# Performance work log

Measured on AMD Instinct MI355X. Metric: run time of the kernel, lower is better.

## Reference

```python
import math
import jax, jax.numpy as jnp
import numpy as np

B, T, C, H = 4, 2048, 1024, 16
HS = C // H


def setup_inputs() -> dict:
    key = jax.random.key(0)
    ks = jax.random.split(key, 5)
    s_in = 1.0 / math.sqrt(C)
    return {
        "x": jax.random.normal(ks[0], (B, T, C), dtype=jnp.float32),
        "w_attn": jax.random.normal(ks[1], (C, 3 * C), dtype=jnp.float32) * s_in,
        "b_attn": jax.random.normal(ks[2], (3 * C,), dtype=jnp.float32) * 0.02,
        "w_proj": jax.random.normal(ks[3], (C, C), dtype=jnp.float32) * s_in,
        "b_proj": jax.random.normal(ks[4], (C,), dtype=jnp.float32) * 0.02,
    }


def reference(x, w_attn, b_attn, w_proj, b_proj):
    Bx, Tx, Cx = x.shape
    hs = Cx // H
    qkv = x @ w_attn + b_attn  # [B, T, 3C]
    q, k, v = jnp.split(qkv, 3, axis=-1)
    # [B, H, T, hs]
    q = q.reshape(Bx, Tx, H, hs).transpose(0, 2, 1, 3)
    k = k.reshape(Bx, Tx, H, hs).transpose(0, 2, 1, 3)
    v = v.reshape(Bx, Tx, H, hs).transpose(0, 2, 1, 3)
    scale = 1.0 / math.sqrt(hs)
    att = jnp.einsum("bhqd,bhkd->bhqk", q, k) * scale  # [B, H, T, T]
    causal = jnp.tril(jnp.ones((Tx, Tx), dtype=bool))
    att = jnp.where(causal, att, -jnp.inf)
    att = jax.nn.softmax(att, axis=-1)
    y = jnp.einsum("bhqk,bhkd->bhqd", att, v)  # [B, H, T, hs]
    y = y.transpose(0, 2, 1, 3).reshape(Bx, Tx, Cx)
    return y @ w_proj + b_proj
```

## Files before the change

kernel.cpp:

```cpp
#include <hip/hip_runtime.h>
#include <stdint.h>

#define Bn 4
#define Tn 2048
#define Cn 1024
#define Hn 16
#define HSn 64
#define Mn (Bn*Tn)
#define N1n (3*Cn)

typedef unsigned short u16;
typedef unsigned int u32;
typedef __attribute__((ext_vector_type(8))) short short8;
typedef __attribute__((ext_vector_type(4))) float f32x4;
typedef __attribute__((ext_vector_type(16))) float f32x16;

__device__ __forceinline__ u16 f2bf(float f){
  u32 u = __float_as_uint(f);
  u += 0x7fffu + ((u >> 16) & 1u);
  return (u16)(u >> 16);
}

__device__ __forceinline__ u32 pkbf(float lo, float hi_){
  u32 r; asm("v_cvt_pk_bf16_f32 %0, %1, %2" : "=v"(r) : "v"(lo), "v"(hi_)); return r;
}

__device__ __forceinline__ float fexp2(float x){
  float r; asm("v_exp_f32 %0, %1" : "=v"(r) : "v"(x)); return r;
}

__device__ __forceinline__ void plswap(u32 &a, u32 &b){
  auto r = __builtin_amdgcn_permlane32_swap(a, b, false, false);
  a = r[0]; b = r[1];
}

__device__ __forceinline__ void gload_lds16(const void* g, void* l){
  __builtin_amdgcn_global_load_lds(
      (const __attribute__((address_space(1))) u32*)g,
      (__attribute__((address_space(3))) u32*)l, 16, 0, 0);
}

#define BARRIER() __builtin_amdgcn_s_barrier()
#define CFENCE() asm volatile("" ::: "memory")

__global__ void k_cvt(const float* __restrict__ in, u16* __restrict__ out, int n8){
  int i = blockIdx.x*256 + threadIdx.x;
  if (i >= n8) return;
  const float4* p = (const float4*)(in) + (size_t)i*2;
  float4 a = p[0], b = p[1];
  uint4 r;
  r.x = (u32)f2bf(a.x) | ((u32)f2bf(a.y) << 16);
  r.y = (u32)f2bf(a.z) | ((u32)f2bf(a.w) << 16);
  r.z = (u32)f2bf(b.x) | ((u32)f2bf(b.y) << 16);
  r.w = (u32)f2bf(b.z) | ((u32)f2bf(b.w) << 16);
  *((uint4*)(out) + i) = r;
}

__global__ void k_tcvt(const float* __restrict__ in, u16* __restrict__ out, int R, int Cc){
  __shared__ float sh[64][68];
  int tid = threadIdx.x;
  int c0 = blockIdx.x*64, r0 = blockIdx.y*64;
  int rr = tid >> 4, c4 = (tid & 15) * 4;
  #pragma unroll
  for (int p=0;p<4;p++){
    int r = rr + 16*p;
    *(float4*)&sh[r][c4] = *(const float4*)&in[(size_t)(r0+r)*Cc + c0 + c4];
  }
  __syncthreads();
  #pragma unroll
  for (int p=0;p<4;p++){
    int oc = rr + 16*p;
    u32 w0 = (u32)f2bf(sh[c4+0][oc]) | ((u32)f2bf(sh[c4+1][oc]) << 16);
    u32 w1 = (u32)f2bf(sh[c4+2][oc]) | ((u32)f2bf(sh[c4+3][oc]) << 16);
    uint2 pk; pk.x = w0; pk.y = w1;
    *(uint2*)&out[(size_t)(c0+oc)*R + r0 + c4] = pk;
  }
}

template <int MODE>
__global__ __launch_bounds__(512, 1)
void k_gemm1p(const u16* __restrict__ A, const u16* __restrict__ Bt,
              const float* __restrict__ bias, void* __restrict__ Cout,
              u16* __restrict__ vt, int Nn_)
{
  extern __shared__ char smem[];
  const int nkt = 16;
  int tid = threadIdx.x;
  int wave = tid >> 6, lane = tid & 63, g = lane >> 4, cl = lane & 15;
  int wm = wave >> 1, wn = wave & 1;

  int blk = blockIdx.x;
  int by = ((blk & 7) << 2) + ((blk >> 3) & 3);
  int bx = ((blk >> 5) & 7) + ((blk >> 8) << 3);
  int m0 = by * 256, n0 = bx * 128;

  int srow = tid >> 3;
  int scolb = (tid & 7) << 4;
  int ssw = scolb ^ ((srow & 7) << 4);
  const char* Agp = (const char*)A  + (size_t)(m0 + srow) * 2048 + ssw;
  const char* Bgp = (const char*)Bt + (size_t)(n0 + srow) * 2048 + ssw;

  #define STAGE6(t_) { int bb_ = (t_)%3; \
    char* ab_ = smem + bb_*32768 + (wave<<10); \
    const char* ag_ = Agp + (size_t)(t_)*128; \
    gload_lds16(ag_,          ab_); \
    gload_lds16(ag_+131072,   ab_+8192); \
    gload_lds16(ag_+262144,   ab_+16384); \
    gload_lds16(ag_+393216,   ab_+24576); \
    char* bbp_ = smem + 98304 + bb_*16384 + (wave<<10); \
    const char* bg_ = Bgp + (size_t)(t_)*128; \
    gload_lds16(bg_,          bbp_); \
    gload_lds16(bg_+131072,   bbp_+8192); }

  f32x4 acc[4][4];
  #pragma unroll
  for (int i=0;i<4;i++)
    #pragma unroll
    for (int j=0;j<4;j++) acc[i][j] = (f32x4){0.f,0.f,0.f,0.f};

  STAGE6(0);
  STAGE6(1);
  asm volatile("s_waitcnt vmcnt(6)" ::: "memory");
  BARRIER(); CFENCE();

  for (int t=0; t<nkt; ++t){
    if (t+2 < nkt){
      STAGE6(t+2);
      asm volatile("s_waitcnt vmcnt(6)" ::: "memory");
    } else {
      asm volatile("s_waitcnt vmcnt(0)" ::: "memory");
    }
    const char* Asb = smem + (t%3)*32768;
    const char* Bsb = smem + 98304 + (t%3)*16384;
    short8 a[4][2], bq[4][2];
    #pragma unroll
    for (int i=0;i<4;i++){
      int row = wm*64 + i*16 + cl;
      #pragma unroll
      for (int ks=0;ks<2;ks++)
        a[i][ks] = *(const short8*)(Asb + row*128 + ((ks*64 + g*16) ^ ((row&7)<<4)));
    }
    #pragma unroll
    for (int j=0;j<4;j++){
      int row = wn*64 + j*16 + cl;
      #pragma unroll
      for (int ks=0;ks<2;ks++)
        bq[j][ks] = *(const short8*)(Bsb + row*128 + ((ks*64 + g*16) ^ ((row&7)<<4)));
    }
    __builtin_amdgcn_s_setprio(1);
    #pragma unroll
    for (int ks=0;ks<2;ks++)
      #pragma unroll
      for (int i=0;i<4;i++)
        #pragma unroll
        for (int j=0;j<4;j++)
          acc[i][j] = __builtin_amdgcn_mfma_f32_16x16x32_bf16(a[i][ks], bq[j][ks], acc[i][j], 0, 0, 0);
    __builtin_amdgcn_s_setprio(0);
    CFENCE(); BARRIER(); CFENCE();
  }
  #undef STAGE6

  #pragma unroll
  for (int jj=0;jj<4;jj++){
    int col = n0 + wn*64 + jj*16 + cl;
    float bj = bias[col];
    if (MODE == 0){
      #pragma unroll
      for (int i=0;i<4;i++){
        int rowb = m0 + wm*64 + i*16 + g*4;
        #pragma unroll
        for (int r=0;r<4;r++)
          ((float*)Cout)[(size_t)(rowb+r)*Nn_ + col] = acc[i][jj][r] + bj;
      }
    } else if (col < 2*Cn){
      #pragma unroll
      for (int i=0;i<4;i++){
        int rowb = m0 + wm*64 + i*16 + g*4;
        #pragma unroll
        for (int r=0;r<4;r++)
          ((u16*)Cout)[(size_t)(rowb+r)*Nn_ + col] = f2bf(acc[i][jj][r] + bj);
      }
    } else {
      int hd = col - 2*Cn;
      #pragma unroll
      for (int i=0;i<4;i++){
        int rowb = m0 + wm*64 + i*16 + g*4;
        int bb = rowb >> 11, tt = rowb & 2047;
        u16* dst = vt + (((size_t)(bb*16 + (hd>>6)))*64 + (hd&63))*2048 + tt;
        uint2 pk;
        pk.x = (u32)f2bf(acc[i][jj][0]+bj) | ((u32)f2bf(acc[i][jj][1]+bj) << 16);
        pk.y = (u32)f2bf(acc[i][jj][2]+bj) | ((u32)f2bf(acc[i][jj][3]+bj) << 16);
        *(uint2*)dst = pk;
      }
    }
  }
}

__global__ __launch_bounds__(256, 4)
void k_attn(const u16* __restrict__ qkv, const u16* __restrict__ vt, u16* __restrict__ yb){
  __shared__ __align__(16) u16 Ks[2][64*64];
  __shared__ __align__(16) u16 Vs[2][64*64];
  int tid = threadIdx.x, wave = tid >> 6, lane = tid & 63;
  int ql = lane & 31, hi = lane >> 5;
  int blk = blockIdx.x;
  int xcd = blk & 7, rest = blk >> 3;
  int bh  = xcd + 8*(rest & 7);
  int qt  = 15 - (rest >> 3);
  int b = bh >> 4, h = bh & 15;

  const u16* Kbase = qkv + (size_t)b*Tn*N1n + Cn + h*HSn;
  const u16* Vbase = vt  + (size_t)bh*HSn*Tn;

  auto STAGE = [&](int bufi, int kt){
    int kb_ = kt*64;
    #pragma unroll
    for (int it=0; it<2; ++it){
      int off = it*4096 + tid*16;
      int row = off >> 7;
      int cb  = off & 127;
      int gc  = (cb ^ ((row & 7) << 4)) >> 1;
      gload_lds16(Kbase + (size_t)(kb_ + row)*N1n + gc,
                  (char*)&Ks[bufi][0] + it*4096 + (wave << 10));
      gload_lds16(Vbase + (size_t)row*Tn + kb_ + gc,
                  (char*)&Vs[bufi][0] + it*4096 + (wave << 10));
    }
  };

  const float QSC = 0.125f * 1.44269504f;

  int q0 = qt * 128;
  int qw0 = q0 + wave*32;
  int qg  = qw0 + ql;
  int ntiles = 2*qt + 2;

  const u16* Qp = qkv + (size_t)(b*Tn + qg)*N1n + h*HSn;
  short8 qf[4];
  #pragma unroll
  for (int dc=0; dc<4; ++dc){
    union { short8 v; u32 w[4]; } qa;
    qa.v = *(const short8*)&Qp[dc*16 + hi*8];
    #pragma unroll
    for (int t=0; t<4; ++t){
      u32 w = qa.w[t];
      float lo = __uint_as_float(w << 16);
      float hf = __uint_as_float(w & 0xffff0000u);
      qa.w[t] = pkbf(lo*QSC, hf*QSC);
    }
    qf[dc] = qa.v;
  }

  f32x16 accO[2];
  #pragma unroll
  for (int f=0; f<2; ++f)
    #pragma unroll
    for (int r=0; r<16; ++r) accO[f][r] = 0.f;
  float m_ = -1e30f, l_ = 0.f;

  STAGE(0, 0);
  asm volatile("s_waitcnt vmcnt(0)" ::: "memory");
  __syncthreads();
  int buf = 0;

  for (int kt=0; kt<ntiles; ++kt){
    if (kt+1 < ntiles) STAGE(buf^1, kt+1);
    const char* Ksb = (const char*)&Ks[buf][0];
    const char* Vsb = (const char*)&Vs[buf][0];
    #pragma unroll
    for (int ksub=0; ksub<2; ++ksub){
      int kbase = kt*64 + ksub*32;
      if (kbase <= qw0 + 31){
        f32x16 s;
        #pragma unroll
        for (int r=0; r<16; ++r) s[r] = 0.f;
        __builtin_amdgcn_s_setprio(1);
        #pragma unroll
        for (int dc=0; dc<4; ++dc){
          short8 kf = *(const short8*)(Ksb + ((ksub*32 + ql) << 7)
                          + ((dc*32 + hi*16) ^ ((ql & 7) << 4)));
          s = __builtin_amdgcn_mfma_f32_32x32x16_bf16(kf, qf[dc], s, 0, 0, 0);
        }
        __builtin_amdgcn_s_setprio(0);
        float p[16];
        if (kbase + 31 > qw0){
          #pragma unroll
          for (int r=0; r<16; ++r){
            int krow = kbase + (r&3) + 8*(r>>2) + 4*hi;
            p[r] = (krow > qg) ? -1e30f : s[r];
          }
        } else {
          #pragma unroll
          for (int r=0; r<16; ++r) p[r] = s[r];
        }
        float t0 = fmaxf(fmaxf(fmaxf(p[0],p[1]),fmaxf(p[2],p[3])),
                         fmaxf(fmaxf(p[4],p[5]),fmaxf(p[6],p[7])));
        float t1 = fmaxf(fmaxf(fmaxf(p[8],p[9]),fmaxf(p[10],p[11])),
                         fmaxf(fmaxf(p[12],p[13]),fmaxf(p[14],p[15])));
        float tm = fmaxf(t0, t1);
        { u32 ua = __float_as_uint(tm), ub = ua; plswap(ua, ub);
          tm = fmaxf(__uint_as_float(ua), __uint_as_float(ub)); }
        if (!__all(tm - m_ <= 8.0f)){
          float mn = fmaxf(m_, tm);
          float al = fexp2(m_ - mn);
          m_ = mn; l_ *= al;
          #pragma unroll
          for (int f=0; f<2; ++f)
            #pragma unroll
            for (int r=0; r<16; ++r) accO[f][r] *= al;
        }
        float ls = 0.f;
        #pragma unroll
        for (int r=0; r<16; ++r){ float e = fexp2(p[r] - m_); p[r] = e; ls += e; }
        { u32 ua = __float_as_uint(ls), ub = ua; plswap(ua, ub);
          l_ += __uint_as_float(ua) + __uint_as_float(ub); }
        #pragma unroll
        for (int ks=0; ks<2; ++ks){
          int pb = ks*8;
          u32 w0 = pkbf(p[pb+0], p[pb+1]);
          u32 w1 = pkbf(p[pb+2], p[pb+3]);
          u32 w2 = pkbf(p[pb+4], p[pb+5]);
          u32 w3 = pkbf(p[pb+6], p[pb+7]);
          plswap(w0, w2);
          plswap(w1, w3);
          union { u32 w[4]; short8 v; } pu;
          pu.w[0] = w0; pu.w[1] = w1; pu.w[2] = w2; pu.w[3] = w3;
          __builtin_amdgcn_s_setprio(1);
          #pragma unroll
          for (int f=0; f<2; ++f){
            short8 vf = *(const short8*)(Vsb + ((f*32 + ql) << 7)
                            + ((ksub*64 + ks*32 + hi*16) ^ ((ql & 7) << 4)));
            accO[f] = __builtin_amdgcn_mfma_f32_32x32x16_bf16(vf, pu.v, accO[f], 0, 0, 0);
          }
          __builtin_amdgcn_s_setprio(0);
        }
      }
    }
    asm volatile("s_waitcnt vmcnt(0)" ::: "memory");
    __syncthreads();
    buf ^= 1;
  }

  float rl = 1.0f / l_;
  u16* yp = yb + (size_t)(b*Tn + qg)*Cn + h*HSn;
  #pragma unroll
  for (int f=0; f<2; ++f)
    #pragma unroll
    for (int rq=0; rq<4; ++rq){
      int d0 = f*32 + rq*8 + hi*4;
      float v0 = accO[f][rq*4+0]*rl, v1 = accO[f][rq*4+1]*rl;
      float v2 = accO[f][rq*4+2]*rl, v3 = accO[f][rq*4+3]*rl;
      uint2 pk2;
      pk2.x = (u32)f2bf(v0) | ((u32)f2bf(v1) << 16);
      pk2.y = (u32)f2bf(v2) | ((u32)f2bf(v3) << 16);
      *(uint2*)&yp[d0] = pk2;
    }
}

extern "C" void kernel_launch(void* const* d_in, const int* in_sizes, int n_in,
                              void* d_out, int out_size, void* d_ws, size_t ws_size,
                              hipStream_t stream)
{
  const float* x      = (const float*)d_in[0];
  const float* w_attn = (const float*)d_in[1];
  const float* b_attn = (const float*)d_in[2];
  const float* w_proj = (const float*)d_in[3];
  const float* b_proj = (const float*)d_in[4];
  float* out = (float*)d_out;
  char* ws = (char*)d_ws;

  size_t off = 0;
  u16* xb  = (u16*)(ws + off); off += (size_t)Mn*Cn*2;
  u16* waT = (u16*)(ws + off); off += (size_t)N1n*Cn*2;
  u16* wpT = (u16*)(ws + off); off += (size_t)Cn*Cn*2;
  u16* qkv = (u16*)(ws + off); off += (size_t)Mn*N1n*2;
  u16* vt  = (u16*)(ws + off); off += (size_t)Bn*Hn*HSn*Tn*2;
  u16* yb  = (u16*)(ws + off); off += (size_t)Mn*Cn*2;

  (void)hipFuncSetAttribute((const void*)k_gemm1p<1>,
        hipFuncAttributeMaxDynamicSharedMemorySize, 147456);
  (void)hipFuncSetAttribute((const void*)k_gemm1p<0>,
        hipFuncAttributeMaxDynamicSharedMemorySize, 147456);

  k_cvt<<<dim3(Mn*Cn/8/256), 256, 0, stream>>>(x, xb, Mn*Cn/8);
  k_tcvt<<<dim3(N1n/64, Cn/64), 256, 0, stream>>>(w_attn, waT, Cn, N1n);
  k_tcvt<<<dim3(Cn/64, Cn/64), 256, 0, stream>>>(w_proj, wpT, Cn, Cn);
  k_gemm1p<1><<<dim3((Mn/256)*(N1n/128)), 512, 147456, stream>>>(xb, waT, b_attn, qkv, vt, N1n);
  k_attn<<<dim3(1024), 256, 0, stream>>>(qkv, vt, yb);
  k_gemm1p<0><<<dim3((Mn/256)*(Cn/128)), 512, 147456, stream>>>(yb, wpT, b_proj, out, nullptr, Cn);
}
```

Measured before the change: 156.7 us.

## Switch GEMMs to 128x128 tiles, 256 threads, double buffering, XCD-aware block mapping

Both GEMMs move from 256x128 tiles on 512-thread blocks with a triple-buffered 144KB LDS pipeline to 128x128 tiles on 256-thread blocks. These use a double-buffered 64KB LDS layout with two blocks per CU. Block indices are remapped so that each XCD owns a contiguous range of M-tiles, which aims for L2 locality, and the grid becomes twice as large. The goal is better occupancy and tail balance, at the cost of a shallower prefetch pipeline, an extra barrier per k-step, and lower per-block data reuse.

```diff
diff --git a/kernel.cpp b/kernel.cpp
--- a/kernel.cpp
+++ b/kernel.cpp
@@ -78,10 +78,10 @@
 }
 
 template <int MODE>
-__global__ __launch_bounds__(512, 1)
-void k_gemm1p(const u16* __restrict__ A, const u16* __restrict__ Bt,
-              const float* __restrict__ bias, void* __restrict__ Cout,
-              u16* __restrict__ vt, int Nn_)
+__global__ __launch_bounds__(256, 2)
+void k_gemm2(const u16* __restrict__ A, const u16* __restrict__ Bt,
+             const float* __restrict__ bias, void* __restrict__ Cout,
+             u16* __restrict__ vt, int Nn_, int byPerXcd)
 {
   extern __shared__ char smem[];
   const int nkt = 16;
@@ -89,10 +89,10 @@
   int wave = tid >> 6, lane = tid & 63, g = lane >> 4, cl = lane & 15;
   int wm = wave >> 1, wn = wave & 1;
 
-  int blk = blockIdx.x;
-  int by = ((blk & 7) << 2) + ((blk >> 3) & 3);
-  int bx = ((blk >> 5) & 7) + ((blk >> 8) << 3);
-  int m0 = by * 256, n0 = bx * 128;
+  int xcd = blockIdx.x & 7, idx = blockIdx.x >> 3;
+  int by = xcd * byPerXcd + (idx % byPerXcd);
+  int bx = idx / byPerXcd;
+  int m0 = by * 128, n0 = bx * 128;
 
   int srow = tid >> 3;
   int scolb = (tid & 7) << 4;
@@ -100,17 +100,19 @@
   const char* Agp = (const char*)A  + (size_t)(m0 + srow) * 2048 + ssw;
   const char* Bgp = (const char*)Bt + (size_t)(n0 + srow) * 2048 + ssw;
 
-  #define STAGE6(t_) { int bb_ = (t_)%3; \
-    char* ab_ = smem + bb_*32768 + (wave<<10); \
-    const char* ag_ = Agp + (size_t)(t_)*128; \
-    gload_lds16(ag_,          ab_); \
-    gload_lds16(ag_+131072,   ab_+8192); \
-    gload_lds16(ag_+262144,   ab_+16384); \
-    gload_lds16(ag_+393216,   ab_+24576); \
-    char* bbp_ = smem + 98304 + bb_*16384 + (wave<<10); \
-    const char* bg_ = Bgp + (size_t)(t_)*128; \
-    gload_lds16(bg_,          bbp_); \
-    gload_lds16(bg_+131072,   bbp_+8192); }
+  #define STG(t_, b_) { \
+    const char* ag = Agp + (size_t)(t_)*128; \
+    const char* bg = Bgp + (size_t)(t_)*128; \
+    char* ab = smem + (b_)*32768 + (wave<<10); \
+    char* bb = ab + 16384; \
+    gload_lds16(ag,          ab); \
+    gload_lds16(ag+ 65536,   ab+4096); \
+    gload_lds16(ag+131072,   ab+8192); \
+    gload_lds16(ag+196608,   ab+12288); \
+    gload_lds16(bg,          bb); \
+    gload_lds16(bg+ 65536,   bb+4096); \
+    gload_lds16(bg+131072,   bb+8192); \
+    gload_lds16(bg+196608,   bb+12288); }
 
   f32x4 acc[4][4];
   #pragma unroll
@@ -118,20 +120,19 @@
     #pragma unroll
     for (int j=0;j<4;j++) acc[i][j] = (f32x4){0.f,0.f,0.f,0.f};
 
-  STAGE6(0);
-  STAGE6(1);
-  asm volatile("s_waitcnt vmcnt(6)" ::: "memory");
-  BARRIER(); CFENCE();
+  STG(0, 0);
 
   for (int t=0; t<nkt; ++t){
-    if (t+2 < nkt){
-      STAGE6(t+2);
-      asm volatile("s_waitcnt vmcnt(6)" ::: "memory");
+    int b = t & 1;
+    if (t+1 < nkt){
+      STG(t+1, b^1);
+      asm volatile("s_waitcnt vmcnt(8)" ::: "memory");
     } else {
       asm volatile("s_waitcnt vmcnt(0)" ::: "memory");
     }
-    const char* Asb = smem + (t%3)*32768;
-    const char* Bsb = smem + 98304 + (t%3)*16384;
+    BARRIER(); CFENCE();
+    const char* Asb = smem + b*32768;
+    const char* Bsb = Asb + 16384;
     short8 a[4][2], bq[4][2];
     #pragma unroll
     for (int i=0;i<4;i++){
@@ -147,6 +148,7 @@
       for (int ks=0;ks<2;ks++)
         bq[j][ks] = *(const short8*)(Bsb + row*128 + ((ks*64 + g*16) ^ ((row&7)<<4)));
     }
+    asm volatile("s_waitcnt lgkmcnt(0)" ::: "memory");
     __builtin_amdgcn_s_setprio(1);
     #pragma unroll
     for (int ks=0;ks<2;ks++)
@@ -158,7 +160,7 @@
     __builtin_amdgcn_s_setprio(0);
     CFENCE(); BARRIER(); CFENCE();
   }
-  #undef STAGE6
+  #undef STG
 
   #pragma unroll
   for (int jj=0;jj<4;jj++){
@@ -375,15 +377,15 @@
   u16* vt  = (u16*)(ws + off); off += (size_t)Bn*Hn*HSn*Tn*2;
   u16* yb  = (u16*)(ws + off); off += (size_t)Mn*Cn*2;
 
-  (void)hipFuncSetAttribute((const void*)k_gemm1p<1>,
-        hipFuncAttributeMaxDynamicSharedMemorySize, 147456);
-  (void)hipFuncSetAttribute((const void*)k_gemm1p<0>,
-        hipFuncAttributeMaxDynamicSharedMemorySize, 147456);
+  (void)hipFuncSetAttribute((const void*)k_gemm2<1>,
+        hipFuncAttributeMaxDynamicSharedMemorySize, 65536);
+  (void)hipFuncSetAttribute((const void*)k_gemm2<0>,
+        hipFuncAttributeMaxDynamicSharedMemorySize, 65536);
 
   k_cvt<<<dim3(Mn*Cn/8/256), 256, 0, stream>>>(x, xb, Mn*Cn/8);
   k_tcvt<<<dim3(N1n/64, Cn/64), 256, 0, stream>>>(w_attn, waT, Cn, N1n);
   k_tcvt<<<dim3(Cn/64, Cn/64), 256, 0, stream>>>(w_proj, wpT, Cn, Cn);
-  k_gemm1p<1><<<dim3((Mn/256)*(N1n/128)), 512, 147456, stream>>>(xb, waT, b_attn, qkv, vt, N1n);
+  k_gemm2<1><<<dim3((Mn/128)*(N1n/128)), 256, 65536, stream>>>(xb, waT, b_attn, qkv, vt, N1n, 8);
   k_attn<<<dim3(1024), 256, 0, stream>>>(qkv, vt, yb);
-  k_gemm1p<0><<<dim3((Mn/256)*(Cn/128)), 512, 147456, stream>>>(yb, wpT, b_proj, out, nullptr, Cn);
-}
+  k_gemm2<0><<<dim3((Mn/128)*(Cn/128)), 256, 65536, stream>>>(yb, wpT, b_proj, out, nullptr, Cn, 8);
+}
```

Result: faster. 148.8 us (-5.1%).
